# Kernel optimization log

Hardware: AMD Instinct MI355X
Metric: run time of the kernel (lower is better)

## Reference

```python
import jax, jax.numpy as jnp
import numpy as np

B, S, D = 4, 2048, 1024
H, DK, DV = 16, 64, 64
NEG = -10000.0
EPS = 1e-5


def setup_inputs() -> dict:
    key = jax.random.key(0)
    ks = jax.random.split(key, 12)
    inp = {
        "q": jax.random.normal(ks[0], (B, S, D), jnp.float32),
        "k": jax.random.normal(ks[1], (B, S, D), jnp.float32),
        "v": jax.random.normal(ks[2], (B, S, D), jnp.float32),
        "mask": jax.random.randint(ks[3], (B, S, S), 0, 2, jnp.int32),
        # linear layers: y = x @ W.T + b (torch convention)
        "Wq": jax.random.normal(ks[4], (H * DK, D), jnp.float32) * (D ** -0.5),
        "bq": jnp.zeros((H * DK,), jnp.float32),
        "Wk": jax.random.normal(ks[5], (H * DK, D), jnp.float32) * (D ** -0.5),
        "bk": jnp.zeros((H * DK,), jnp.float32),
        "Wv": jax.random.normal(ks[6], (H * DV, D), jnp.float32) * (D ** -0.5),
        "bv": jnp.zeros((H * DV,), jnp.float32),
        "ln_g": jnp.ones((D,), jnp.float32),
        "ln_b": jnp.zeros((D,), jnp.float32),
    }
    return inp


def reference(q, k, v, mask, Wq, bq, Wk, bk, Wv, bv, ln_g, ln_b):
    residual = q
    # project and split heads -> [B, H, S, dk]
    qh = (q @ Wq.T + bq).reshape(B, S, H, DK).transpose(0, 2, 1, 3)
    kh = (k @ Wk.T + bk).reshape(B, S, H, DK).transpose(0, 2, 1, 3)
    vh = (v @ Wv.T + bv).reshape(B, S, H, DV).transpose(0, 2, 1, 3)

    scale = DK ** -0.5
    attn = jnp.einsum("bhqd,bhkd->bhqk", qh * scale, kh)  # [B,H,S,S]
    # padding mask adder: (1 - mask) * -1e4, broadcast over heads
    attn = attn + (1.0 - mask.astype(attn.dtype))[:, None, :, :] * NEG
    # causal mask adder
    causal = jnp.tril(jnp.ones((S, S), attn.dtype))
    attn = attn + (1.0 - causal) * NEG
    attn = jax.nn.softmax(attn, axis=-1)

    out = jnp.einsum("bhqk,bhkd->bhqd", attn, vh)  # [B,H,S,dv]
    out = out.transpose(0, 2, 1, 3).reshape(B, S, H * DV)
    out = out + residual
    # layer norm (eps=1e-5)
    mu = jnp.mean(out, axis=-1, keepdims=True)
    var = jnp.mean(jnp.square(out - mu), axis=-1, keepdims=True)
    out = (out - mu) * jax.lax.rsqrt(var + EPS) * ln_g + ln_b
    return out, attn
```

## Files before the change

kernel.cpp:

```cpp
#include <hip/hip_runtime.h>

typedef __bf16 bf16;
typedef float f32x4 __attribute__((ext_vector_type(4)));
typedef bf16 bf16x8 __attribute__((ext_vector_type(8)));
typedef bf16 bf16x4 __attribute__((ext_vector_type(4)));

constexpr int Bc = 4, Sc = 2048, Dc = 1024, Hc = 16, DKc = 64;
constexpr float NEGc = -10000.0f;

__global__ __launch_bounds__(256, 2) void proj_kernel(
    const float* __restrict__ xq, const float* __restrict__ xk, const float* __restrict__ xv,
    const float* __restrict__ Wq, const float* __restrict__ bq,
    const float* __restrict__ Wk, const float* __restrict__ bk,
    const float* __restrict__ Wv, const float* __restrict__ bv,
    bf16* __restrict__ qh, bf16* __restrict__ kh, bf16* __restrict__ vh)
{
    const int z = blockIdx.z;
    const float* x    = (z == 0) ? xq : (z == 1) ? xk : xv;
    const float* W    = (z == 0) ? Wq : (z == 1) ? Wk : Wv;
    const float* bias = (z == 0) ? bq : (z == 1) ? bk : bv;
    bf16* dst         = (z == 0) ? qh : (z == 1) ? kh : vh;

    const int tid = threadIdx.x;
    const int wave = tid >> 6, lane = tid & 63, quad = lane >> 4, m16 = lane & 15;
    const int wm = (wave >> 1) * 64, wn = (wave & 1) * 64;
    const int m0 = blockIdx.y * 128, n0 = blockIdx.x * 128;

    __shared__ bf16 As[128][40];
    __shared__ bf16 Bs[128][40];

    const f32x4 zero4 = {0.f, 0.f, 0.f, 0.f};
    f32x4 acc[4][4];
#pragma unroll
    for (int i = 0; i < 4; i++)
#pragma unroll
        for (int j = 0; j < 4; j++) acc[i][j] = zero4;

    for (int kk = 0; kk < 32; ++kk) {
        const int k0 = kk * 32;
#pragma unroll
        for (int i = 0; i < 4; i++) {
            int f4 = tid + i * 256;
            int r = f4 >> 3, c4 = (f4 & 7) * 4;
            float4 a = *(const float4*)&x[(size_t)(m0 + r) * Dc + k0 + c4];
            float4 w = *(const float4*)&W[(size_t)(n0 + r) * Dc + k0 + c4];
            bf16x4 av; av.x = (bf16)a.x; av.y = (bf16)a.y; av.z = (bf16)a.z; av.w = (bf16)a.w;
            bf16x4 wv; wv.x = (bf16)w.x; wv.y = (bf16)w.y; wv.z = (bf16)w.z; wv.w = (bf16)w.w;
            *(bf16x4*)&As[r][c4] = av;
            *(bf16x4*)&Bs[r][c4] = wv;
        }
        __syncthreads();
        bf16x8 af[4], bfr[4];
#pragma unroll
        for (int t = 0; t < 4; t++) {
            af[t]  = *(const bf16x8*)&As[wm + t * 16 + m16][quad * 8];
            bfr[t] = *(const bf16x8*)&Bs[wn + t * 16 + m16][quad * 8];
        }
#pragma unroll
        for (int mt = 0; mt < 4; mt++)
#pragma unroll
            for (int nt = 0; nt < 4; nt++)
                acc[mt][nt] = __builtin_amdgcn_mfma_f32_16x16x32_bf16(af[mt], bfr[nt], acc[mt][nt], 0, 0, 0);
        __syncthreads();
    }

#pragma unroll
    for (int nt = 0; nt < 4; nt++) {
        int n = n0 + wn + nt * 16 + m16;
        float bval = bias[n];
        int h = n >> 6, d = n & 63;
#pragma unroll
        for (int mt = 0; mt < 4; mt++) {
#pragma unroll
            for (int r = 0; r < 4; r++) {
                int m = m0 + wm + mt * 16 + quad * 4 + r;
                int bb = m >> 11, s = m & 2047;
                float val = acc[mt][nt][r] + bval;
                dst[(((size_t)(bb * Hc + h)) * Sc + s) * DKc + d] = (bf16)val;
            }
        }
    }
}

__global__ __launch_bounds__(256) void vtrans_kernel(const bf16* __restrict__ vh,
                                                     bf16* __restrict__ vt)
{
    const int tid = threadIdx.x;
    const int bh = blockIdx.y, s0 = blockIdx.x * 64;
    __shared__ bf16 tile[64][72];
    const bf16* src = vh + ((size_t)bh * Sc + s0) * DKc;
#pragma unroll
    for (int i = 0; i < 2; i++) {
        int v = tid + i * 256;
        int sl = v >> 3, d8 = (v & 7) * 8;
        *(bf16x8*)&tile[sl][d8] = *(const bf16x8*)&src[sl * DKc + d8];
    }
    __syncthreads();
#pragma unroll
    for (int i = 0; i < 2; i++) {
        int v = tid + i * 256;
        int d = v >> 3, s8 = (v & 7) * 8;
        bf16x8 o;
#pragma unroll
        for (int j = 0; j < 8; j++) o[j] = tile[s8 + j][d];
        *(bf16x8*)&vt[((size_t)bh * DKc + d) * Sc + s0 + s8] = o;
    }
}

__global__ __launch_bounds__(256, 2) void attn_kernel(
    const bf16* __restrict__ qh, const bf16* __restrict__ kh, const bf16* __restrict__ vt,
    const int* __restrict__ mask, float* __restrict__ attn_out, float* __restrict__ out)
{
    const int qtr = (int)gridDim.x - 1 - (int)blockIdx.x;
    const int h = blockIdx.y, b = blockIdx.z;
    const int bh = b * Hc + h, q0 = qtr * 16;
    const int tid = threadIdx.x;
    const int wave = tid >> 6, lane = tid & 63, quad = lane >> 4, m16 = lane & 15;

    __shared__ bf16 sc[16][256];
    __shared__ float red[128];

    const bf16* qrow = qh + ((size_t)bh * Sc + q0) * DKc;
    const bf16* krow = kh + (size_t)bh * Sc * DKc;
    const bf16* vrow = vt + (size_t)bh * DKc * Sc;
    const int*  mrow = mask + (size_t)b * Sc * Sc;

    const bf16x8 aq0 = *(const bf16x8*)&qrow[m16 * DKc + quad * 8];
    const bf16x8 aq1 = *(const bf16x8*)&qrow[m16 * DKc + 32 + quad * 8];

    const f32x4 zero4 = {0.f, 0.f, 0.f, 0.f};
    f32x4 acc[32];
#pragma unroll
    for (int t = 0; t < 32; t++) acc[t] = zero4;

    const int gq = qtr >> 4;

#pragma unroll
    for (int g = 0; g < 8; g++) {
        if (g <= gq) {
#pragma unroll
            for (int tp = 0; tp < 4; tp++) {
                const int t = g * 4 + tp;
                const int n0 = (t * 4 + wave) * 16;
                const bf16* kb = &krow[(size_t)(n0 + m16) * DKc + quad * 8];
                bf16x8 b0 = *(const bf16x8*)kb;
                bf16x8 b1 = *(const bf16x8*)(kb + 32);
                acc[t] = __builtin_amdgcn_mfma_f32_16x16x32_bf16(aq0, b0, acc[t], 0, 0, 0);
                acc[t] = __builtin_amdgcn_mfma_f32_16x16x32_bf16(aq1, b1, acc[t], 0, 0, 0);
            }
        }
    }

    float rmax[4] = {-3e38f, -3e38f, -3e38f, -3e38f};
#pragma unroll
    for (int t = 0; t < 32; t++) {
        const int j = t * 4 + wave;
        if (j <= qtr) {
            const int kcol = j * 16 + m16;
#pragma unroll
            for (int r = 0; r < 4; r++) {
                const int grow = q0 + quad * 4 + r;
                const int mv = mrow[(size_t)grow * Sc + kcol];
                float s = acc[t][r] * 0.125f;
                s += (mv == 0) ? NEGc : 0.f;
                s += (kcol > grow) ? NEGc : 0.f;
                acc[t][r] = s;
                rmax[r] = fmaxf(rmax[r], s);
            }
        }
    }
#pragma unroll
    for (int off = 1; off < 16; off <<= 1)
#pragma unroll
        for (int r = 0; r < 4; r++) rmax[r] = fmaxf(rmax[r], __shfl_xor(rmax[r], off, 64));
    if (m16 == 0) {
#pragma unroll
        for (int r = 0; r < 4; r++) red[wave * 16 + quad * 4 + r] = rmax[r];
    }
    __syncthreads();
#pragma unroll
    for (int r = 0; r < 4; r++) {
        const int row = quad * 4 + r;
        rmax[r] = fmaxf(fmaxf(red[row], red[16 + row]), fmaxf(red[32 + row], red[48 + row]));
    }

    float mn = fminf(fminf(rmax[0], rmax[1]), fminf(rmax[2], rmax[3]));
    mn = fminf(mn, __shfl_xor(mn, 16, 64));
    mn = fminf(mn, __shfl_xor(mn, 32, 64));
    const bool needfull = (mn <= -5000.0f);
    int Jmax = qtr;

    if (needfull) {
        __syncthreads();
#pragma unroll
        for (int g = 0; g < 8; g++) {
            if (g > gq) {
#pragma unroll
                for (int tp = 0; tp < 4; tp++) {
                    const int t = g * 4 + tp;
                    const int n0 = (t * 4 + wave) * 16;
                    const bf16* kb = &krow[(size_t)(n0 + m16) * DKc + quad * 8];
                    bf16x8 b0 = *(const bf16x8*)kb;
                    bf16x8 b1 = *(const bf16x8*)(kb + 32);
                    acc[t] = __builtin_amdgcn_mfma_f32_16x16x32_bf16(aq0, b0, acc[t], 0, 0, 0);
                    acc[t] = __builtin_amdgcn_mfma_f32_16x16x32_bf16(aq1, b1, acc[t], 0, 0, 0);
                }
            }
        }
#pragma unroll
        for (int t = 0; t < 32; t++) {
            const int j = t * 4 + wave;
            if (j > qtr) {
                const int kcol = j * 16 + m16;
#pragma unroll
                for (int r = 0; r < 4; r++) {
                    const int grow = q0 + quad * 4 + r;
                    const int mv = mrow[(size_t)grow * Sc + kcol];
                    float s = acc[t][r] * 0.125f;
                    s += (mv == 0) ? NEGc : 0.f;
                    s += (kcol > grow) ? NEGc : 0.f;
                    acc[t][r] = s;
                    rmax[r] = fmaxf(rmax[r], s);
                }
            }
        }
#pragma unroll
        for (int off = 1; off < 16; off <<= 1)
#pragma unroll
            for (int r = 0; r < 4; r++) rmax[r] = fmaxf(rmax[r], __shfl_xor(rmax[r], off, 64));
        if (m16 == 0) {
#pragma unroll
            for (int r = 0; r < 4; r++) red[wave * 16 + quad * 4 + r] = rmax[r];
        }
        __syncthreads();
#pragma unroll
        for (int r = 0; r < 4; r++) {
            const int row = quad * 4 + r;
            rmax[r] = fmaxf(fmaxf(red[row], red[16 + row]), fmaxf(red[32 + row], red[48 + row]));
        }
        Jmax = 127;
    }

    float rsum[4] = {0.f, 0.f, 0.f, 0.f};
#pragma unroll
    for (int t = 0; t < 32; t++) {
        const int j = t * 4 + wave;
        if (j <= Jmax) {
#pragma unroll
            for (int r = 0; r < 4; r++) {
                float e = __expf(acc[t][r] - rmax[r]);
                acc[t][r] = e;
                rsum[r] += e;
            }
        }
    }
#pragma unroll
    for (int off = 1; off < 16; off <<= 1)
#pragma unroll
        for (int r = 0; r < 4; r++) rsum[r] += __shfl_xor(rsum[r], off, 64);
    if (m16 == 0) {
#pragma unroll
        for (int r = 0; r < 4; r++) red[64 + wave * 16 + quad * 4 + r] = rsum[r];
    }
    __syncthreads();
    float inv[4];
#pragma unroll
    for (int r = 0; r < 4; r++) {
        const int row = quad * 4 + r;
        inv[r] = 1.0f / (red[64 + row] + red[80 + row] + red[96 + row] + red[112 + row]);
    }

    float* arow_base = attn_out + ((size_t)bh * Sc + q0) * Sc;
#pragma unroll
    for (int t = 0; t < 32; t++) {
        const int j = t * 4 + wave;
        if (j <= Jmax) {
            const int kcol = j * 16 + m16;
#pragma unroll
            for (int r = 0; r < 4; r++) {
                const int row = quad * 4 + r;
                const float p = acc[t][r] * inv[r];
                acc[t][r] = p;
                __builtin_nontemporal_store(p, &arow_base[(size_t)row * Sc + kcol]);
            }
        }
    }
    if (!needfull) {
        const int z0 = (qtr + 1) * 16;
        const int c4n = (Sc - z0) >> 2;
#pragma unroll
        for (int r = 0; r < 16; r++) {
            float* rp = arow_base + (size_t)r * Sc + z0;
            for (int c = tid; c < c4n; c += 256)
                __builtin_nontemporal_store(zero4, (f32x4*)(rp + 4 * c));
        }
    }

    const int dcol = wave * 16 + m16;
    const bf16* vbase = &vrow[(size_t)dcol * Sc];
    const int swz = (m16 & 7) << 3;
    f32x4 oacc = zero4;
#pragma unroll
    for (int c = 0; c < 8; c++) {
        if (c * 16 <= Jmax) {
            __syncthreads();
#pragma unroll
            for (int tp = 0; tp < 4; tp++) {
                const int t = c * 4 + tp;
                const int j = t * 4 + wave;
                const int lc = (tp * 4 + wave) * 16 + m16;
                if (j <= Jmax) {
#pragma unroll
                    for (int r = 0; r < 4; r++) {
                        const int row = quad * 4 + r;
                        sc[row][lc ^ ((row & 7) << 3)] = (bf16)acc[t][r];
                    }
                } else if (j <= (Jmax | 1)) {
#pragma unroll
                    for (int r = 0; r < 4; r++) {
                        const int row = quad * 4 + r;
                        sc[row][lc ^ ((row & 7) << 3)] = (bf16)0.f;
                    }
                }
            }
            __syncthreads();
#pragma unroll
            for (int lks = 0; lks < 8; lks++) {
                if (c * 16 + 2 * lks <= Jmax) {
                    const int k0 = lks * 32 + quad * 8;
                    bf16x8 a  = *(const bf16x8*)&sc[m16][k0 ^ swz];
                    bf16x8 b8 = *(const bf16x8*)&vbase[c * 256 + k0];
                    oacc = __builtin_amdgcn_mfma_f32_16x16x32_bf16(a, b8, oacc, 0, 0, 0);
                }
            }
        }
    }
    float* obase = out + ((size_t)(b * Sc + q0)) * Dc + h * DKc;
#pragma unroll
    for (int r = 0; r < 4; r++) {
        const int row = quad * 4 + r;
        obase[(size_t)row * Dc + dcol] = oacc[r];
    }
}

__global__ __launch_bounds__(256) void ln_kernel(float* __restrict__ out,
                                                 const float* __restrict__ resid,
                                                 const float* __restrict__ gw,
                                                 const float* __restrict__ bw)
{
    const int row = blockIdx.x, tid = threadIdx.x;
    float* orow = out + (size_t)row * Dc;
    const float* rrow = resid + (size_t)row * Dc;
    float4 x = *(const float4*)&orow[tid * 4];
    float4 rr = *(const float4*)&rrow[tid * 4];
    x.x += rr.x; x.y += rr.y; x.z += rr.z; x.w += rr.w;
    float s1 = x.x + x.y + x.z + x.w;
    float s2 = x.x * x.x + x.y * x.y + x.z * x.z + x.w * x.w;
#pragma unroll
    for (int off = 1; off < 64; off <<= 1) {
        s1 += __shfl_xor(s1, off, 64);
        s2 += __shfl_xor(s2, off, 64);
    }
    __shared__ float red[8];
    const int wave = tid >> 6, lane = tid & 63;
    if (lane == 0) { red[wave] = s1; red[4 + wave] = s2; }
    __syncthreads();
    s1 = red[0] + red[1] + red[2] + red[3];
    s2 = red[4] + red[5] + red[6] + red[7];
    const float mu = s1 * (1.f / Dc);
    const float var = s2 * (1.f / Dc) - mu * mu;
    const float rstd = rsqrtf(var + 1e-5f);
    float4 g4 = *(const float4*)&gw[tid * 4];
    float4 b4 = *(const float4*)&bw[tid * 4];
    float4 y;
    y.x = (x.x - mu) * rstd * g4.x + b4.x;
    y.y = (x.y - mu) * rstd * g4.y + b4.y;
    y.z = (x.z - mu) * rstd * g4.z + b4.z;
    y.w = (x.w - mu) * rstd * g4.w + b4.w;
    *(float4*)&orow[tid * 4] = y;
}

extern "C" void kernel_launch(void* const* d_in, const int* in_sizes, int n_in,
                              void* d_out, int out_size, void* d_ws, size_t ws_size,
                              hipStream_t stream)
{
    (void)in_sizes; (void)n_in; (void)out_size; (void)ws_size;
    const float* q    = (const float*)d_in[0];
    const float* k    = (const float*)d_in[1];
    const float* v    = (const float*)d_in[2];
    const int*   mask = (const int*)d_in[3];
    const float* Wq   = (const float*)d_in[4];
    const float* bq   = (const float*)d_in[5];
    const float* Wk   = (const float*)d_in[6];
    const float* bk   = (const float*)d_in[7];
    const float* Wv   = (const float*)d_in[8];
    const float* bv   = (const float*)d_in[9];
    const float* g    = (const float*)d_in[10];
    const float* bet  = (const float*)d_in[11];

    float* out  = (float*)d_out;
    float* attn = out + (size_t)Bc * Sc * Dc;

    const size_t headN = (size_t)Bc * Hc * Sc * DKc;
    bf16* qh = (bf16*)d_ws;
    bf16* kh = qh + headN;
    bf16* vh = kh + headN;
    bf16* vt = vh + headN;

    proj_kernel<<<dim3(8, 64, 3), 256, 0, stream>>>(q, k, v, Wq, bq, Wk, bk, Wv, bv, qh, kh, vh);
    vtrans_kernel<<<dim3(Sc / 64, Bc * Hc), 256, 0, stream>>>(vh, vt);
    attn_kernel<<<dim3(Sc / 16, Hc, Bc), 256, 0, stream>>>(qh, kh, vt, mask, attn, out);
    ln_kernel<<<dim3(Bc * Sc), 256, 0, stream>>>(out, q, g, bet);
}
```

Before: 1.667 ms.

## Pre-convert inputs to bf16, pack mask to bytes, fuse attn store into PV loop

Adds a kernel that converts the activations and weights to bf16 once, staging them in the attn output buffer, so the projection GEMM loads half the bytes and does no conversions. A pack kernel turns each int32 padding mask row into a per-lane-permuted byte array in the workspace. The attention kernel then reads each lane's mask bytes with a few wide loads instead of scattered int32 loads, but only when the workspace is large enough. The normalized probabilities are now written inside the PV loop using double-buffered LDS, and the zero-fill of the masked tail moves to the end of the kernel. The extra conversion and pack passes add memory traffic and launches, and the mask words add register pressure.

```diff
diff --git a/kernel.cpp b/kernel.cpp
--- a/kernel.cpp
+++ b/kernel.cpp
@@ -4,20 +4,68 @@
 typedef float f32x4 __attribute__((ext_vector_type(4)));
 typedef bf16 bf16x8 __attribute__((ext_vector_type(8)));
 typedef bf16 bf16x4 __attribute__((ext_vector_type(4)));
+typedef unsigned int u32;
+typedef unsigned char u8;
 
 constexpr int Bc = 4, Sc = 2048, Dc = 1024, Hc = 16, DKc = 64;
 constexpr float NEGc = -10000.0f;
 
-__global__ __launch_bounds__(256, 2) void proj_kernel(
+__global__ __launch_bounds__(256) void cvt_kernel(
     const float* __restrict__ xq, const float* __restrict__ xk, const float* __restrict__ xv,
-    const float* __restrict__ Wq, const float* __restrict__ bq,
-    const float* __restrict__ Wk, const float* __restrict__ bk,
-    const float* __restrict__ Wv, const float* __restrict__ bv,
+    const float* __restrict__ Wq, const float* __restrict__ Wk, const float* __restrict__ Wv,
+    bf16* __restrict__ xbq, bf16* __restrict__ xbk, bf16* __restrict__ xbv,
+    bf16* __restrict__ wbq, bf16* __restrict__ wbk, bf16* __restrict__ wbv)
+{
+    const int z = blockIdx.y;
+    const float* src = (z == 0) ? xq : (z == 1) ? xk : (z == 2) ? xv
+                      : (z == 3) ? Wq : (z == 4) ? Wk : Wv;
+    bf16* dst = (z == 0) ? xbq : (z == 1) ? xbk : (z == 2) ? xbv
+               : (z == 3) ? wbq : (z == 4) ? wbk : wbv;
+    const int n4 = ((z < 3) ? (Bc * Sc * Dc) : (Dc * Dc)) >> 2;
+    const int stride = gridDim.x * 256;
+    for (int i = blockIdx.x * 256 + threadIdx.x; i < n4; i += stride) {
+        float4 v = ((const float4*)src)[i];
+        bf16x4 o; o.x = (bf16)v.x; o.y = (bf16)v.y; o.z = (bf16)v.z; o.w = (bf16)v.w;
+        ((bf16x4*)dst)[i] = o;
+    }
+}
+
+__global__ __launch_bounds__(256) void pack_kernel(const int* __restrict__ mask,
+                                                   u8* __restrict__ mp)
+{
+    const int row = blockIdx.x;
+    const int tid = threadIdx.x;
+    __shared__ u8 lm[2048];
+    const int4* src = (const int4*)(mask + (size_t)row * Sc);
+#pragma unroll
+    for (int i = 0; i < 2; i++) {
+        int4 v = src[tid * 2 + i];
+        const int o = tid * 8 + i * 4;
+        lm[o + 0] = (u8)(v.x != 0); lm[o + 1] = (u8)(v.y != 0);
+        lm[o + 2] = (u8)(v.z != 0); lm[o + 3] = (u8)(v.w != 0);
+    }
+    __syncthreads();
+    u32 w0 = 0, w1 = 0;
+#pragma unroll
+    for (int i = 0; i < 8; i++) {
+        const int o = tid * 8 + i;
+        const int m16 = o >> 7, wv = (o >> 5) & 3, t = o & 31;
+        const u32 bv = lm[(t * 4 + wv) * 16 + m16];
+        if (i < 4) w0 |= bv << (8 * i); else w1 |= bv << (8 * (i - 4));
+    }
+    ((uint2*)(mp + (size_t)row * 2048))[tid] = make_uint2(w0, w1);
+}
+
+__global__ __launch_bounds__(256, 2) void projb_kernel(
+    const bf16* __restrict__ xq, const bf16* __restrict__ xk, const bf16* __restrict__ xv,
+    const bf16* __restrict__ Wq, const float* __restrict__ bq,
+    const bf16* __restrict__ Wk, const float* __restrict__ bk,
+    const bf16* __restrict__ Wv, const float* __restrict__ bv,
     bf16* __restrict__ qh, bf16* __restrict__ kh, bf16* __restrict__ vh)
 {
     const int z = blockIdx.z;
-    const float* x    = (z == 0) ? xq : (z == 1) ? xk : xv;
-    const float* W    = (z == 0) ? Wq : (z == 1) ? Wk : Wv;
+    const bf16* x     = (z == 0) ? xq : (z == 1) ? xk : xv;
+    const bf16* W     = (z == 0) ? Wq : (z == 1) ? Wk : Wv;
     const float* bias = (z == 0) ? bq : (z == 1) ? bk : bv;
     bf16* dst         = (z == 0) ? qh : (z == 1) ? kh : vh;
 
@@ -39,15 +87,11 @@
     for (int kk = 0; kk < 32; ++kk) {
         const int k0 = kk * 32;
 #pragma unroll
-        for (int i = 0; i < 4; i++) {
-            int f4 = tid + i * 256;
-            int r = f4 >> 3, c4 = (f4 & 7) * 4;
-            float4 a = *(const float4*)&x[(size_t)(m0 + r) * Dc + k0 + c4];
-            float4 w = *(const float4*)&W[(size_t)(n0 + r) * Dc + k0 + c4];
-            bf16x4 av; av.x = (bf16)a.x; av.y = (bf16)a.y; av.z = (bf16)a.z; av.w = (bf16)a.w;
-            bf16x4 wv; wv.x = (bf16)w.x; wv.y = (bf16)w.y; wv.z = (bf16)w.z; wv.w = (bf16)w.w;
-            *(bf16x4*)&As[r][c4] = av;
-            *(bf16x4*)&Bs[r][c4] = wv;
+        for (int i = 0; i < 2; i++) {
+            int v8 = tid + i * 256;
+            int r = v8 >> 2, c8 = (v8 & 3) * 8;
+            *(bf16x8*)&As[r][c8] = *(const bf16x8*)&x[(size_t)(m0 + r) * Dc + k0 + c8];
+            *(bf16x8*)&Bs[r][c8] = *(const bf16x8*)&W[(size_t)(n0 + r) * Dc + k0 + c8];
         }
         __syncthreads();
         bf16x8 af[4], bfr[4];
@@ -107,9 +151,11 @@
     }
 }
 
+template<bool PACKED>
 __global__ __launch_bounds__(256, 2) void attn_kernel(
     const bf16* __restrict__ qh, const bf16* __restrict__ kh, const bf16* __restrict__ vt,
-    const int* __restrict__ mask, float* __restrict__ attn_out, float* __restrict__ out)
+    const int* __restrict__ mask, const u8* __restrict__ mp,
+    float* __restrict__ attn_out, float* __restrict__ out)
 {
     const int qtr = (int)gridDim.x - 1 - (int)blockIdx.x;
     const int h = blockIdx.y, b = blockIdx.z;
@@ -117,16 +163,27 @@
     const int tid = threadIdx.x;
     const int wave = tid >> 6, lane = tid & 63, quad = lane >> 4, m16 = lane & 15;
 
-    __shared__ bf16 sc[16][256];
+    __shared__ bf16 sc[2][16][256];
     __shared__ float red[128];
 
     const bf16* qrow = qh + ((size_t)bh * Sc + q0) * DKc;
     const bf16* krow = kh + (size_t)bh * Sc * DKc;
     const bf16* vrow = vt + (size_t)bh * DKc * Sc;
-    const int*  mrow = mask + (size_t)b * Sc * Sc;
 
     const bf16x8 aq0 = *(const bf16x8*)&qrow[m16 * DKc + quad * 8];
     const bf16x8 aq1 = *(const bf16x8*)&qrow[m16 * DKc + 32 + quad * 8];
+
+    u32 mw[4][8];
+    if constexpr (PACKED) {
+#pragma unroll
+        for (int r = 0; r < 4; r++) {
+            const int grow = q0 + quad * 4 + r;
+            const u8* p = mp + ((size_t)b * Sc + grow) * 2048 + m16 * 128 + wave * 32;
+            uint4 a = *(const uint4*)p, c = *(const uint4*)(p + 16);
+            mw[r][0] = a.x; mw[r][1] = a.y; mw[r][2] = a.z; mw[r][3] = a.w;
+            mw[r][4] = c.x; mw[r][5] = c.y; mw[r][6] = c.z; mw[r][7] = c.w;
+        }
+    }
 
     const f32x4 zero4 = {0.f, 0.f, 0.f, 0.f};
     f32x4 acc[32];
@@ -160,9 +217,14 @@
 #pragma unroll
             for (int r = 0; r < 4; r++) {
                 const int grow = q0 + quad * 4 + r;
-                const int mv = mrow[(size_t)grow * Sc + kcol];
-                float s = acc[t][r] * 0.125f;
-                s += (mv == 0) ? NEGc : 0.f;
+                float s;
+                if constexpr (PACKED) {
+                    const float bf = (float)((mw[r][t >> 2] >> ((t & 3) * 8)) & 0xffu);
+                    s = fmaf(bf, 10000.0f, NEGc) + acc[t][r] * 0.125f;
+                } else {
+                    const int mv = mask[((size_t)b * Sc + grow) * Sc + kcol];
+                    s = acc[t][r] * 0.125f + ((mv == 0) ? NEGc : 0.f);
+                }
                 s += (kcol > grow) ? NEGc : 0.f;
                 acc[t][r] = s;
                 rmax[r] = fmaxf(rmax[r], s);
@@ -215,9 +277,14 @@
 #pragma unroll
                 for (int r = 0; r < 4; r++) {
                     const int grow = q0 + quad * 4 + r;
-                    const int mv = mrow[(size_t)grow * Sc + kcol];
-                    float s = acc[t][r] * 0.125f;
-                    s += (mv == 0) ? NEGc : 0.f;
+                    float s;
+                    if constexpr (PACKED) {
+                        const float bf = (float)((mw[r][t >> 2] >> ((t & 3) * 8)) & 0xffu);
+                        s = fmaf(bf, 10000.0f, NEGc) + acc[t][r] * 0.125f;
+                    } else {
+                        const int mv = mask[((size_t)b * Sc + grow) * Sc + kcol];
+                        s = acc[t][r] * 0.125f + ((mv == 0) ? NEGc : 0.f);
+                    }
                     s += (kcol > grow) ? NEGc : 0.f;
                     acc[t][r] = s;
                     rmax[r] = fmaxf(rmax[r], s);
@@ -270,56 +337,34 @@
         inv[r] = 1.0f / (red[64 + row] + red[80 + row] + red[96 + row] + red[112 + row]);
     }
 
-    float* arow_base = attn_out + ((size_t)bh * Sc + q0) * Sc;
-#pragma unroll
-    for (int t = 0; t < 32; t++) {
-        const int j = t * 4 + wave;
-        if (j <= Jmax) {
-            const int kcol = j * 16 + m16;
-#pragma unroll
-            for (int r = 0; r < 4; r++) {
-                const int row = quad * 4 + r;
-                const float p = acc[t][r] * inv[r];
-                acc[t][r] = p;
-                __builtin_nontemporal_store(p, &arow_base[(size_t)row * Sc + kcol]);
-            }
-        }
-    }
-    if (!needfull) {
-        const int z0 = (qtr + 1) * 16;
-        const int c4n = (Sc - z0) >> 2;
-#pragma unroll
-        for (int r = 0; r < 16; r++) {
-            float* rp = arow_base + (size_t)r * Sc + z0;
-            for (int c = tid; c < c4n; c += 256)
-                __builtin_nontemporal_store(zero4, (f32x4*)(rp + 4 * c));
-        }
-    }
-
     const int dcol = wave * 16 + m16;
     const bf16* vbase = &vrow[(size_t)dcol * Sc];
     const int swz = (m16 & 7) << 3;
+    float* arow_base = attn_out + ((size_t)bh * Sc + q0) * Sc;
     f32x4 oacc = zero4;
 #pragma unroll
     for (int c = 0; c < 8; c++) {
         if (c * 16 <= Jmax) {
-            __syncthreads();
+            const int cb = c & 1;
 #pragma unroll
             for (int tp = 0; tp < 4; tp++) {
                 const int t = c * 4 + tp;
                 const int j = t * 4 + wave;
                 const int lc = (tp * 4 + wave) * 16 + m16;
                 if (j <= Jmax) {
+                    const int kcol = j * 16 + m16;
 #pragma unroll
                     for (int r = 0; r < 4; r++) {
                         const int row = quad * 4 + r;
-                        sc[row][lc ^ ((row & 7) << 3)] = (bf16)acc[t][r];
+                        const float p = acc[t][r] * inv[r];
+                        __builtin_nontemporal_store(p, &arow_base[(size_t)row * Sc + kcol]);
+                        sc[cb][row][lc ^ ((row & 7) << 3)] = (bf16)p;
                     }
                 } else if (j <= (Jmax | 1)) {
 #pragma unroll
                     for (int r = 0; r < 4; r++) {
                         const int row = quad * 4 + r;
-                        sc[row][lc ^ ((row & 7) << 3)] = (bf16)0.f;
+                        sc[cb][row][lc ^ ((row & 7) << 3)] = (bf16)0.f;
                     }
                 }
             }
@@ -328,7 +373,7 @@
             for (int lks = 0; lks < 8; lks++) {
                 if (c * 16 + 2 * lks <= Jmax) {
                     const int k0 = lks * 32 + quad * 8;
-                    bf16x8 a  = *(const bf16x8*)&sc[m16][k0 ^ swz];
+                    bf16x8 a  = *(const bf16x8*)&sc[cb][m16][k0 ^ swz];
                     bf16x8 b8 = *(const bf16x8*)&vbase[c * 256 + k0];
                     oacc = __builtin_amdgcn_mfma_f32_16x16x32_bf16(a, b8, oacc, 0, 0, 0);
                 }
@@ -340,6 +385,17 @@
     for (int r = 0; r < 4; r++) {
         const int row = quad * 4 + r;
         obase[(size_t)row * Dc + dcol] = oacc[r];
+    }
+
+    if (!needfull) {
+        const int z0 = (qtr + 1) * 16;
+        const int c4n = (Sc - z0) >> 2;
+#pragma unroll
+        for (int r = 0; r < 16; r++) {
+            float* rp = arow_base + (size_t)r * Sc + z0;
+            for (int c = tid; c < c4n; c += 256)
+                __builtin_nontemporal_store(zero4, (f32x4*)(rp + 4 * c));
+        }
     }
 }
 
@@ -384,7 +440,7 @@
                               void* d_out, int out_size, void* d_ws, size_t ws_size,
                               hipStream_t stream)
 {
-    (void)in_sizes; (void)n_in; (void)out_size; (void)ws_size;
+    (void)in_sizes; (void)n_in; (void)out_size;
     const float* q    = (const float*)d_in[0];
     const float* k    = (const float*)d_in[1];
     const float* v    = (const float*)d_in[2];
@@ -406,9 +462,26 @@
     bf16* kh = qh + headN;
     bf16* vh = kh + headN;
     bf16* vt = vh + headN;
-
-    proj_kernel<<<dim3(8, 64, 3), 256, 0, stream>>>(q, k, v, Wq, bq, Wk, bk, Wv, bv, qh, kh, vh);
+    u8*   mp = (u8*)(vt + headN);
+    const bool packed = ws_size >= 4 * headN * sizeof(bf16) + (size_t)Bc * Sc * Sc;
+
+    const size_t XN = (size_t)Bc * Sc * Dc;
+    bf16* xbq = (bf16*)attn;
+    bf16* xbk = xbq + XN;
+    bf16* xbv = xbk + XN;
+    bf16* wbq = xbv + XN;
+    bf16* wbk = wbq + (size_t)Dc * Dc;
+    bf16* wbv = wbk + (size_t)Dc * Dc;
+
+    cvt_kernel<<<dim3(1024, 6), 256, 0, stream>>>(q, k, v, Wq, Wk, Wv,
+                                                  xbq, xbk, xbv, wbq, wbk, wbv);
+    if (packed) pack_kernel<<<dim3(Bc * Sc), 256, 0, stream>>>(mask, mp);
+    projb_kernel<<<dim3(8, 64, 3), 256, 0, stream>>>(xbq, xbk, xbv, wbq, bq, wbk, bk, wbv, bv,
+                                                     qh, kh, vh);
     vtrans_kernel<<<dim3(Sc / 64, Bc * Hc), 256, 0, stream>>>(vh, vt);
-    attn_kernel<<<dim3(Sc / 16, Hc, Bc), 256, 0, stream>>>(qh, kh, vt, mask, attn, out);
+    if (packed)
+        attn_kernel<true><<<dim3(Sc / 16, Hc, Bc), 256, 0, stream>>>(qh, kh, vt, mask, mp, attn, out);
+    else
+        attn_kernel<false><<<dim3(Sc / 16, Hc, Bc), 256, 0, stream>>>(qh, kh, vt, mask, mp, attn, out);
     ln_kernel<<<dim3(Bc * Sc), 256, 0, stream>>>(out, q, g, bet);
 }
```

Result: faster. 1.583 ms (-5.0%).
